# Kernel tuning notes

Hardware: AMD Instinct MI355X
Metric: run time of the kernel (lower is better)

The kernel has to match this reference:

```python
import jax, jax.numpy as jnp
import numpy as np
from jax import lax

DEPTH, HEADS, DH, DIM, M, V, NUM_EMB, D_VQ = 6, 8, 64, 512, 256, 523, 512, 64


def _ln(x, g, b):
    mu = jnp.mean(x, -1, keepdims=True)
    var = jnp.var(x, -1, keepdims=True)
    return (x - mu) * lax.rsqrt(var + 1e-5) * g + b


def _softmax_kernel(data, proj, is_query):
    # FAVOR+ positive softmax features (performer-pytorch softmax_kernel)
    dn = data * (data.shape[-1] ** -0.25)
    dd = jnp.einsum('bhld,md->bhlm', dn, proj)
    diag = 0.5 * jnp.sum(dn * dn, axis=-1, keepdims=True)
    mx = jnp.max(dd, axis=-1, keepdims=True) if is_query else jnp.max(dd)
    return jnp.exp(dd - diag - lax.stop_gradient(mx)) * (proj.shape[0] ** -0.5) + 1e-4


def _causal_linear_attn(qp, kp, v):
    # out_t = qp_t . cumsum_t(kp v^T) / (qp_t . cumsum_t(kp))
    kc = jnp.cumsum(kp, axis=2)
    den = jnp.einsum('bhlm,bhlm->bhl', qp, kc)
    kv = jnp.cumsum(jnp.einsum('bhlm,bhld->bhlmd', kp, v), axis=2)
    return jnp.einsum('bhlm,bhlmd->bhld', qp, kv) / den[..., None]


def _vq_encode(_x, conv1_w, conv1_b, conv2_w, conv2_b, codebook):
    dn = ('NCDHW', 'OIDHW', 'NCDHW')
    h = lax.conv_general_dilated(_x, conv1_w, (2, 2, 2), [(1, 1)] * 3, dimension_numbers=dn)
    h = jax.nn.relu(h + conv1_b[None, :, None, None, None])
    h = lax.conv_general_dilated(h, conv2_w, (2, 2, 2), [(1, 1)] * 3, dimension_numbers=dn)
    h = h + conv2_b[None, :, None, None, None]                 # [N, D, 4,4,4]
    z = jnp.transpose(h, (0, 2, 3, 4, 1))                      # [N, 4,4,4, D]
    flat = z.reshape(-1, z.shape[-1])
    d2 = (jnp.sum(flat * flat, 1, keepdims=True)
          - 2.0 * flat @ codebook.T
          + jnp.sum(codebook * codebook, 1)[None, :])
    inds = jnp.argmin(d2, axis=1).astype(jnp.int32)
    return inds.reshape(z.shape[:4])                           # [N, 4,4,4]


def _performer_loss(seq, tok_emb, pos_emb, proj, ln1_g, ln1_b, wq, wk, wv, wo, bo,
                    ln2_g, ln2_b, ff1_w, ff1_b, ff2_w, ff2_b, lnf_g, lnf_b,
                    logits_w, logits_b):
    inp, tgt = seq[:, :-1], seq[:, 1:]
    b, L = inp.shape
    h = tok_emb[inp] + pos_emb[:L][None]
    split = lambda t: jnp.transpose(t.reshape(b, L, HEADS, DH), (0, 2, 1, 3))
    for l in range(DEPTH):
        x1 = _ln(h, ln1_g[l], ln1_b[l])
        q, k, v = split(x1 @ wq[l]), split(x1 @ wk[l]), split(x1 @ wv[l])
        qp = _softmax_kernel(q, proj[l], True)
        kp = _softmax_kernel(k, proj[l], False)
        o = _causal_linear_attn(qp, kp, v)
        o = jnp.transpose(o, (0, 2, 1, 3)).reshape(b, L, DIM)
        h = h + o @ wo[l] + bo[l]
        x2 = _ln(h, ln2_g[l], ln2_b[l])
        h = h + jax.nn.gelu(x2 @ ff1_w[l] + ff1_b[l]) @ ff2_w[l] + ff2_b[l]
    h = _ln(h, lnf_g, lnf_b)
    logits = h @ logits_w + logits_b
    lp = jax.nn.log_softmax(logits, axis=-1)
    nll = -jnp.take_along_axis(lp, tgt[..., None], axis=-1)[..., 0]
    return jnp.mean(nll)


def setup_inputs() -> dict:
    key = jax.random.key(0)
    ks = jax.random.split(key, 24)
    n = lambda k, sh, s=0.02: (jax.random.normal(k, sh) * s).astype(jnp.float32)
    bs = 16
    return {
        'x': jax.random.normal(ks[0], (bs, 1, 16, 16, 16), jnp.float32),
        'xn': jax.random.normal(ks[1], (bs, 1, 1, 16, 16, 16), jnp.float32),
        'i': jax.random.randint(ks[2], (bs, 3), 0, V, jnp.int32),
        # frozen VQ-VAE
        'conv1_w': n(ks[3], (32, 1, 4, 4, 4), 0.1), 'conv1_b': jnp.zeros((32,), jnp.float32),
        'conv2_w': n(ks[4], (D_VQ, 32, 4, 4, 4), 0.05), 'conv2_b': jnp.zeros((D_VQ,), jnp.float32),
        'codebook': jax.random.normal(ks[5], (NUM_EMB, D_VQ), jnp.float32),
        # FAVOR+ random-feature projections (non-trainable buffer)
        'proj': jax.random.normal(ks[6], (DEPTH, M, DH), jnp.float32),
        # performer params
        'tok_emb': n(ks[7], (V, DIM)), 'pos_emb': n(ks[8], (131, DIM)),
        'ln1_g': jnp.ones((DEPTH, DIM), jnp.float32), 'ln1_b': jnp.zeros((DEPTH, DIM), jnp.float32),
        'wq': n(ks[9], (DEPTH, DIM, DIM)), 'wk': n(ks[10], (DEPTH, DIM, DIM)),
        'wv': n(ks[11], (DEPTH, DIM, DIM)), 'wo': n(ks[12], (DEPTH, DIM, DIM)),
        'bo': jnp.zeros((DEPTH, DIM), jnp.float32),
        'ln2_g': jnp.ones((DEPTH, DIM), jnp.float32), 'ln2_b': jnp.zeros((DEPTH, DIM), jnp.float32),
        'ff1_w': n(ks[13], (DEPTH, DIM, 4 * DIM)), 'ff1_b': jnp.zeros((DEPTH, 4 * DIM), jnp.float32),
        'ff2_w': n(ks[14], (DEPTH, 4 * DIM, DIM)), 'ff2_b': jnp.zeros((DEPTH, DIM), jnp.float32),
        'lnf_g': jnp.ones((DIM,), jnp.float32), 'lnf_b': jnp.zeros((DIM,), jnp.float32),
        'logits_w': n(ks[15], (DIM, V)), 'logits_b': jnp.zeros((V,), jnp.float32),
    }


def reference(x, xn, i, conv1_w, conv1_b, conv2_w, conv2_b, codebook, proj,
              tok_emb, pos_emb, ln1_g, ln1_b, wq, wk, wv, wo, bo, ln2_g, ln2_b,
              ff1_w, ff1_b, ff2_w, ff2_b, lnf_g, lnf_b, logits_w, logits_b):
    bs = x.shape[0]
    _xn = xn.reshape((-1,) + xn.shape[2:])            # (b n) c x y z
    _x = jnp.concatenate([x, _xn], axis=0)
    inds = _vq_encode(_x, conv1_w, conv1_b, conv2_w, conv2_b, codebook)
    inds_i = inds[:bs].reshape(bs, -1)                # b (x y z)
    inds_r = inds[bs:].reshape(bs, -1)                # b (n x y z)
    seq = jnp.concatenate([i.astype(jnp.int32), inds_r, inds_i], axis=1)  # [b, 131]
    return _performer_loss(seq, tok_emb, pos_emb, proj, ln1_g, ln1_b, wq, wk, wv, wo,
                           bo, ln2_g, ln2_b, ff1_w, ff1_b, ff2_w, ff2_b,
                           lnf_g, lnf_b, logits_w, logits_b)
```

## Files before the change

kernel.cpp:

```cpp
#include <hip/hip_runtime.h>

#define SEQL 130
#define LSEQ 131
#define DIMM 512
#define NHEADS 8
#define MF 256
#define VSZ 523
#define NROWS (16*SEQL)
#define NBH (16*NHEADS)
#define NBHL (NBH*SEQL)
#define QSEG 1064960

typedef __attribute__((ext_vector_type(8))) short short8;
typedef __attribute__((ext_vector_type(8))) unsigned short us8;
typedef __attribute__((ext_vector_type(4))) unsigned short us4;
typedef __attribute__((ext_vector_type(4))) float f32x4;

__device__ __forceinline__ unsigned short f2bf(float f){
  unsigned int u = __float_as_uint(f);
  u += 0x7fffu + ((u>>16)&1u);
  return (unsigned short)(u>>16);
}
__device__ __forceinline__ float bf2f(unsigned short h){
  return __uint_as_float(((unsigned int)h)<<16);
}
__device__ __forceinline__ float gelu_f(float x){
  float x3 = x*x*x;
  return 0.5f*x*(1.f+tanhf(0.7978845608028654f*(x+0.044715f*x3)));
}
__device__ __forceinline__ unsigned enc_max(float f){
  unsigned u = __float_as_uint(f);
  return (u & 0x80000000u) ? ~u : (u | 0x80000000u);
}
__device__ __forceinline__ float dec_max(unsigned k){
  unsigned u = (k>>31) ? (k & 0x7fffffffu) : ~k;
  return __uint_as_float(u);
}
__device__ __forceinline__ float blk_sum(float v){
  #pragma unroll
  for(int off=32;off;off>>=1) v += __shfl_xor(v,off);
  __shared__ float tmp_s[4];
  int t=threadIdx.x;
  if((t&63)==0) tmp_s[t>>6]=v;
  __syncthreads();
  v = tmp_s[0]+tmp_s[1]+tmp_s[2]+tmp_s[3];
  __syncthreads();
  return v;
}
__device__ __forceinline__ float blk_max(float v){
  #pragma unroll
  for(int off=32;off;off>>=1) v = fmaxf(v,__shfl_xor(v,off));
  __shared__ float tmp_m[4];
  int t=threadIdx.x;
  if((t&63)==0) tmp_m[t>>6]=v;
  __syncthreads();
  v = fmaxf(fmaxf(tmp_m[0],tmp_m[1]),fmaxf(tmp_m[2],tmp_m[3]));
  __syncthreads();
  return v;
}
__device__ __forceinline__ int tok_at(const int* __restrict__ iarr,
    const int* __restrict__ inds, int b, int p){
  if(p<3)  return iarr[b*3+p];
  if(p<67) return inds[(16+b)*64 + (p-3)];
  return inds[b*64 + (p-67)];
}

__global__ __launch_bounds__(256) void conv1_k(const float* __restrict__ x,
    const float* __restrict__ xn, const float* __restrict__ w,
    const float* __restrict__ bias, float* __restrict__ out){
  int idx = blockIdx.x*256 + threadIdx.x;
  if(idx >= 32*32*8*8*8) return;
  int ow = idx & 7, oh = (idx>>3)&7, od = (idx>>6)&7, oc = (idx>>9)&31, n = idx>>14;
  const float* xp = (n<16) ? (x + n*4096) : (xn + (n-16)*4096);
  const float* wp = w + oc*64;
  float acc = bias[oc];
  #pragma unroll
  for(int kd=0;kd<4;kd++){ int id = od*2-1+kd; if((unsigned)id>=16u) continue;
    #pragma unroll
    for(int kh=0;kh<4;kh++){ int ih = oh*2-1+kh; if((unsigned)ih>=16u) continue;
      #pragma unroll
      for(int kw=0;kw<4;kw++){ int iw = ow*2-1+kw; if((unsigned)iw>=16u) continue;
        acc += xp[(id*16+ih)*16+iw]*wp[(kd*4+kh)*4+kw];
      }}}
  out[idx] = fmaxf(acc,0.f);
}

__global__ __launch_bounds__(256) void cvt8_k(const float* __restrict__ src,
    unsigned short* __restrict__ dst, int n8){
  int i = blockIdx.x*256 + threadIdx.x;
  if(i >= n8) return;
  const float* s = src + (size_t)i*8;
  us8 u;
  #pragma unroll
  for(int j=0;j<8;j++) u[j] = f2bf(s[j]);
  *(us8*)(dst + (size_t)i*8) = u;
}

__global__ __launch_bounds__(256) void im2col_k(const float* __restrict__ c1,
    unsigned short* __restrict__ icol){
  int tid = blockIdx.x*256 + threadIdx.x;
  size_t e0 = (size_t)tid*8;
  int r = (int)(e0 >> 11);
  int k0 = (int)(e0 & 2047);
  int n = r>>6, od = (r>>4)&3, oh = (r>>2)&3, ow = r&3;
  int ic = k0>>6, kd = (k0>>4)&3, kh0 = (k0>>2)&3;
  int id = od*2 - 1 + kd;
  us8 u = {};
  if((unsigned)id < 8u){
    const float* base = c1 + (size_t)(n*32+ic)*512 + id*64;
    #pragma unroll
    for(int j=0;j<8;j++){
      int kh = kh0 + (j>>2), kw = j&3;
      int ih = oh*2 - 1 + kh, iw = ow*2 - 1 + kw;
      float v = 0.f;
      if((unsigned)ih < 8u && (unsigned)iw < 8u) v = base[ih*8 + iw];
      u[j] = f2bf(v);
    }
  }
  *(us8*)(icol + e0) = u;
}

__global__ __launch_bounds__(256) void vq_k(const float* __restrict__ z,
    const float* __restrict__ cb, int* __restrict__ inds){
  int nf = blockIdx.x;
  __shared__ float zs[64];
  int t = threadIdx.x;
  if(t<64) zs[t] = z[(size_t)nf*64 + t];
  __syncthreads();
  float best = 3.0e38f; int bi = 0;
  for(int j=t; j<512; j+=256){
    const float* cr = cb + j*64;
    float dot=0.f, nn=0.f;
    #pragma unroll 8
    for(int d=0;d<64;d++){ float cv=cr[d]; dot += zs[d]*cv; nn += cv*cv; }
    float dist = nn - 2.f*dot;
    if(dist < best){ best=dist; bi=j; }
  }
  #pragma unroll
  for(int off=32;off;off>>=1){
    float ob = __shfl_down(best,off); int oi = __shfl_down(bi,off);
    if(ob<best || (ob==best && oi<bi)){ best=ob; bi=oi; }
  }
  __shared__ float rb[4]; __shared__ int ri[4];
  if((t&63)==0){ rb[t>>6]=best; ri[t>>6]=bi; }
  __syncthreads();
  if(t==0){
    for(int wv=1;wv<4;wv++){ if(rb[wv]<best || (rb[wv]==best && ri[wv]<bi)){ best=rb[wv]; bi=ri[wv]; } }
    inds[nf]=bi;
  }
}

__global__ __launch_bounds__(256) void embed_k(const int* __restrict__ iarr,
    const int* __restrict__ inds, const float* __restrict__ tok,
    const float* __restrict__ pos, float* __restrict__ h){
  int idx = blockIdx.x*256 + threadIdx.x;
  int c = idx & 511; int row = idx >> 9;
  int b = row/SEQL, l = row - b*SEQL;
  int tk = tok_at(iarr, inds, b, l);
  h[idx] = tok[tk*DIMM + c] + pos[l*DIMM + c];
}

__global__ __launch_bounds__(256) void ln_k(const float* __restrict__ in,
    const float* __restrict__ g, const float* __restrict__ bb,
    unsigned short* __restrict__ out){
  int row = blockIdx.x; int t = threadIdx.x;
  const float* xr = in + (size_t)row*DIMM;
  float x0 = xr[t], x1 = xr[t+256];
  float s = x0+x1, ss = x0*x0 + x1*x1;
  #pragma unroll
  for(int off=32;off;off>>=1){ s += __shfl_xor(s,off); ss += __shfl_xor(ss,off); }
  __shared__ float bs[4], bss[4];
  if((t&63)==0){ bs[t>>6]=s; bss[t>>6]=ss; }
  __syncthreads();
  s = bs[0]+bs[1]+bs[2]+bs[3]; ss = bss[0]+bss[1]+bss[2]+bss[3];
  float mu = s*(1.f/512.f);
  float var = ss*(1.f/512.f) - mu*mu;
  float inv = rsqrtf(var + 1e-5f);
  out[(size_t)row*DIMM+t]     = f2bf((x0-mu)*inv*g[t]     + bb[t]);
  out[(size_t)row*DIMM+t+256] = f2bf((x1-mu)*inv*g[t+256] + bb[t+256]);
}

__global__ __launch_bounds__(256) void wprep_k(const float* __restrict__ wq_l,
    const float* __restrict__ wk_l, const float* __restrict__ wv_l,
    const float* __restrict__ wo_l, const float* __restrict__ ff1_l,
    const float* __restrict__ ff2_l,
    unsigned short* __restrict__ wqkvt, unsigned short* __restrict__ wot,
    unsigned short* __restrict__ ff1t, unsigned short* __restrict__ ff2t,
    unsigned int* __restrict__ gmaxbits){
  int bid = blockIdx.x;
  int t = threadIdx.x;
  if(bid==0 && t==0) gmaxbits[0] = 0u;
  const float* src; unsigned short* dst;
  int n0, k0, srcN, dstK;
  if(bid < 768){
    int nt = bid % 48, kt = bid / 48;
    n0 = nt*32; k0 = kt*32;
    int seg = n0 >> 9;
    src = (seg==0 ? wq_l : seg==1 ? wk_l : wv_l);
    dst = wqkvt; srcN = 512; dstK = 512;
  } else if(bid < 1024){
    int b2 = bid-768; int nt = b2 % 16, kt = b2 / 16;
    n0 = nt*32; k0 = kt*32; src = wo_l; dst = wot; srcN = 512; dstK = 512;
  } else if(bid < 2048){
    int b2 = bid-1024; int nt = b2 % 64, kt = b2 / 64;
    n0 = nt*32; k0 = kt*32; src = ff1_l; dst = ff1t; srcN = 2048; dstK = 512;
  } else {
    int b2 = bid-2048; int nt = b2 % 16, kt = b2 / 16;
    n0 = nt*32; k0 = kt*32; src = ff2_l; dst = ff2t; srcN = 512; dstK = 2048;
  }
  int srcCol0 = (bid < 768) ? (n0 & 0x1ff) : n0;
  __shared__ float tile[32][33];
  int c = t&31, r = t>>5;
  #pragma unroll
  for(int j=0;j<4;j++)
    tile[r+8*j][c] = src[(size_t)(k0+r+8*j)*srcN + srcCol0 + c];
  __syncthreads();
  #pragma unroll
  for(int j=0;j<4;j++){
    int n = n0 + r + 8*j;
    dst[(size_t)n*dstK + k0 + c] = f2bf(tile[c][r+8*j]);
  }
}

__global__ __launch_bounds__(256) void wconv_k(const float* __restrict__ W,
    unsigned short* __restrict__ dst, int K, int N){
  __shared__ float tile[32][33];
  int k0 = blockIdx.y*32, n0 = blockIdx.x*32;
  int t = threadIdx.x; int c = t&31, r = t>>5;
  #pragma unroll
  for(int j=0;j<4;j++){
    int n = n0+c;
    tile[r+8*j][c] = (n<N) ? W[(size_t)(k0+r+8*j)*N + n] : 0.f;
  }
  __syncthreads();
  #pragma unroll
  for(int j=0;j<4;j++){
    int n = n0 + r + 8*j;
    if(n<N) dst[(size_t)n*K + k0 + c] = f2bf(tile[c][r+8*j]);
  }
}

template<int MODE>
__global__ __launch_bounds__(256) void mgemm_k(const unsigned short* __restrict__ A,
    const unsigned short* __restrict__ Bt, const float* __restrict__ bias,
    float* __restrict__ Cf, unsigned short* __restrict__ Cb,
    int M, int N, int K){
  __shared__ unsigned short As[4096];
  __shared__ unsigned short Bs[4096];
  int t = threadIdx.x;
  const int m0 = blockIdx.y*64, n0 = blockIdx.x*64;
  int w = t>>6, l = t&63;
  int wr = w>>1, wc = w&1;
  f32x4 acc[2][2] = {};
  int srow = t>>2, sp = (t&3)*2;
  int arow = m0 + srow, brow = n0 + srow;
  bool aok = arow < M, bok = brow < N;
  const us8* Ap = (const us8*)(A + (size_t)arow*K + sp*8);
  const us8* Bp = (const us8*)(Bt + (size_t)brow*K + sp*8);
  unsigned short* Aw0 = As + srow*64 + (((sp  )^(srow&7))<<3);
  unsigned short* Aw1 = As + srow*64 + (((sp+1)^(srow&7))<<3);
  unsigned short* Bw0 = Bs + srow*64 + (((sp  )^(srow&7))<<3);
  unsigned short* Bw1 = Bs + srow*64 + (((sp+1)^(srow&7))<<3);
  for(int k0=0; k0<K; k0+=64){
    us8 a0={}, a1={}, b0={}, b1={};
    if(aok){ a0 = Ap[0]; a1 = Ap[1]; }
    if(bok){ b0 = Bp[0]; b1 = Bp[1]; }
    Ap += 8; Bp += 8;
    __syncthreads();
    *(us8*)Aw0 = a0; *(us8*)Aw1 = a1;
    *(us8*)Bw0 = b0; *(us8*)Bw1 = b1;
    __syncthreads();
    #pragma unroll
    for(int kk=0;kk<2;kk++){
      short8 af[2], bf[2];
      #pragma unroll
      for(int m=0;m<2;m++){
        int row = wr*32 + m*16 + (l&15);
        int slot = kk*4 + (l>>4);
        af[m] = *(const short8*)(As + row*64 + ((slot^(row&7))<<3));
      }
      #pragma unroll
      for(int n=0;n<2;n++){
        int col = wc*32 + n*16 + (l&15);
        int slot = kk*4 + (l>>4);
        bf[n] = *(const short8*)(Bs + col*64 + ((slot^(col&7))<<3));
      }
      #pragma unroll
      for(int m=0;m<2;m++)
        #pragma unroll
        for(int n=0;n<2;n++)
          acc[m][n] = __builtin_amdgcn_mfma_f32_16x16x32_bf16(af[m], bf[n], acc[m][n], 0, 0, 0);
    }
  }
  #pragma unroll
  for(int m=0;m<2;m++){
    #pragma unroll
    for(int n=0;n<2;n++){
      int col = n0 + wc*32 + n*16 + (l&15);
      #pragma unroll
      for(int i=0;i<4;i++){
        int row = m0 + wr*32 + m*16 + (l>>4)*4 + i;
        if(row < M && col < N){
          float v = acc[m][n][i];
          if(MODE==0){
            if(bias) v += bias[col];
            Cf[(size_t)row*N+col] = v;
          } else if(MODE==1){
            v *= (col < 1024) ? 0.35355339059327378f : 1.0f;
            int seg = col>>9, d0 = col&511;
            int hh = d0>>6, d = d0&63;
            int bb = row/SEQL, ll = row - bb*SEQL;
            Cb[(size_t)seg*QSEG + (((size_t)(bb*NHEADS+hh))*SEQL + ll)*64 + d] = f2bf(v);
          } else if(MODE==3){
            v += bias[col];
            Cf[(size_t)row*N+col] += v;
          } else {
            v += bias[col];
            v = gelu_f(v);
            Cb[(size_t)row*N+col] = f2bf(v);
          }
        }
      }
    }
  }
}

template<int ACC>
__global__ __launch_bounds__(256) void mgemm32_k(const unsigned short* __restrict__ A,
    const unsigned short* __restrict__ Bt, const float* __restrict__ bias,
    float* __restrict__ Cf, int N, int K){
  __shared__ unsigned short As[2048];
  __shared__ unsigned short Bs[4096];
  int t = threadIdx.x;
  const int m0 = blockIdx.y*32, n0 = blockIdx.x*64;
  int w = t>>6, l = t&63;
  int wm = w&1, wn2 = w>>1;
  f32x4 acc[2] = {};
  int srowA = t>>3, spA = t&7;
  int srowB = t>>2, spB = (t&3)*2;
  const us8* Ap = (const us8*)(A + (size_t)(m0+srowA)*K + spA*8);
  const us8* Bp = (const us8*)(Bt + (size_t)(n0+srowB)*K + spB*8);
  unsigned short* Aw  = As + srowA*64 + ((spA^(srowA&7))<<3);
  unsigned short* Bw0 = Bs + srowB*64 + (((spB  )^(srowB&7))<<3);
  unsigned short* Bw1 = Bs + srowB*64 + (((spB+1)^(srowB&7))<<3);
  for(int k0=0; k0<K; k0+=64){
    us8 a0 = Ap[0];
    us8 b0 = Bp[0], b1 = Bp[1];
    Ap += 8; Bp += 8;
    __syncthreads();
    *(us8*)Aw = a0;
    *(us8*)Bw0 = b0; *(us8*)Bw1 = b1;
    __syncthreads();
    #pragma unroll
    for(int kk=0;kk<2;kk++){
      int arow = wm*16 + (l&15);
      int slot = kk*4 + (l>>4);
      short8 af = *(const short8*)(As + arow*64 + ((slot^(arow&7))<<3));
      #pragma unroll
      for(int n=0;n<2;n++){
        int col = (wn2*2+n)*16 + (l&15);
        short8 bf = *(const short8*)(Bs + col*64 + ((slot^(col&7))<<3));
        acc[n] = __builtin_amdgcn_mfma_f32_16x16x32_bf16(af, bf, acc[n], 0, 0, 0);
      }
    }
  }
  #pragma unroll
  for(int n=0;n<2;n++){
    int col = n0 + (wn2*2+n)*16 + (l&15);
    float bv = bias[col];
    #pragma unroll
    for(int i=0;i<4;i++){
      int row = m0 + wm*16 + (l>>4)*4 + i;
      if(ACC) Cf[(size_t)row*N+col] += acc[n][i] + bv;
      else    Cf[(size_t)row*N+col]  = acc[n][i] + bv;
    }
  }
}

__global__ __launch_bounds__(256) void featA_k(const unsigned short* __restrict__ qn,
    const unsigned short* __restrict__ kn, const unsigned short* __restrict__ projl,
    unsigned short* __restrict__ qp, unsigned int* __restrict__ gmaxbits){
  int z = blockIdx.y;
  const unsigned short* dn = z ? kn : qn;
  __shared__ float uni[32*264];
  __shared__ unsigned short dns[2048];
  unsigned short* ps = (unsigned short*)uni;
  int t = threadIdx.x;
  size_t R0 = (size_t)blockIdx.x*32;
  {
    int row = t>>3, sl = t&7;
    us8 u = *(const us8*)(dn + (R0+row)*64 + sl*8);
    *(us8*)(dns + row*64 + ((sl^(row&7))<<3)) = u;
  }
  #pragma unroll
  for(int j=0;j<8;j++){
    int ridx = t + 256*j;
    int row = ridx>>3, sl = ridx&7;
    us8 u = *(const us8*)(projl + row*64 + sl*8);
    *(us8*)(ps + row*64 + ((sl^(row&7))<<3)) = u;
  }
  __syncthreads();
  int w = t>>6, l = t&63;
  int rt = w&1, cb = (w>>1)*8;
  f32x4 acc[8] = {};
  #pragma unroll
  for(int kk=0;kk<2;kk++){
    int ar = rt*16 + (l&15);
    int slot = kk*4 + (l>>4);
    short8 a = *(const short8*)(dns + ar*64 + ((slot^(ar&7))<<3));
    #pragma unroll
    for(int ct=0;ct<8;ct++){
      int br = (cb+ct)*16 + (l&15);
      short8 b = *(const short8*)(ps + br*64 + ((slot^(br&7))<<3));
      acc[ct] = __builtin_amdgcn_mfma_f32_16x16x32_bf16(a, b, acc[ct], 0, 0, 0);
    }
  }
  __syncthreads();
  #pragma unroll
  for(int ct=0;ct<8;ct++){
    int col = (cb+ct)*16 + (l&15);
    #pragma unroll
    for(int i=0;i<4;i++){
      int row = rt*16 + (l>>4)*4 + i;
      uni[row*264 + col] = acc[ct][i];
    }
  }
  __syncthreads();
  int r = t>>3, sub = t&7;
  float* rowp = uni + r*264 + sub*32;
  f32x4 v[8];
  #pragma unroll
  for(int jj=0;jj<8;jj++) v[jj] = *(const f32x4*)(rowp + jj*4);
  float m = -3.0e38f;
  #pragma unroll
  for(int jj=0;jj<8;jj++)
    #pragma unroll
    for(int i=0;i<4;i++) m = fmaxf(m, v[jj][i]);
  m = fmaxf(m, __shfl_xor(m,1));
  m = fmaxf(m, __shfl_xor(m,2));
  m = fmaxf(m, __shfl_xor(m,4));
  if(z==0){
    us8 dvu = *(const us8*)(dns + r*64 + ((sub^(r&7))<<3));
    float s2 = 0.f;
    #pragma unroll
    for(int j=0;j<8;j++){ float xx = bf2f(dvu[j]); s2 += xx*xx; }
    s2 += __shfl_xor(s2,1); s2 += __shfl_xor(s2,2); s2 += __shfl_xor(s2,4);
    float ds = 0.5f*s2;
    unsigned short* op = qp + (R0+r)*256 + sub*32;
    #pragma unroll
    for(int jj=0;jj<8;jj++){
      us4 u4;
      #pragma unroll
      for(int i=0;i<4;i++) u4[i] = f2bf(expf(v[jj][i] - ds - m)*0.0625f + 1e-4f);
      *(us4*)(op + jj*4) = u4;
    }
  } else {
    float bm = m;
    bm = fmaxf(bm, __shfl_xor(bm,8));
    bm = fmaxf(bm, __shfl_xor(bm,16));
    bm = fmaxf(bm, __shfl_xor(bm,32));
    __shared__ float wm[4];
    if(l==0) wm[w] = bm;
    __syncthreads();
    if(t==0){
      float g = fmaxf(fmaxf(wm[0],wm[1]),fmaxf(wm[2],wm[3]));
      atomicMax(gmaxbits, enc_max(g));
    }
  }
}

__global__ __launch_bounds__(256) void featB_k(const unsigned short* __restrict__ kn,
    const unsigned short* __restrict__ projl, const unsigned int* __restrict__ gmaxbits,
    unsigned short* __restrict__ kp){
  __shared__ float uni[32*264];
  __shared__ unsigned short dns[2048];
  unsigned short* ps = (unsigned short*)uni;
  int t = threadIdx.x;
  size_t R0 = (size_t)blockIdx.x*32;
  {
    int row = t>>3, sl = t&7;
    us8 u = *(const us8*)(kn + (R0+row)*64 + sl*8);
    *(us8*)(dns + row*64 + ((sl^(row&7))<<3)) = u;
  }
  #pragma unroll
  for(int j=0;j<8;j++){
    int ridx = t + 256*j;
    int row = ridx>>3, sl = ridx&7;
    us8 u = *(const us8*)(projl + row*64 + sl*8);
    *(us8*)(ps + row*64 + ((sl^(row&7))<<3)) = u;
  }
  __syncthreads();
  int w = t>>6, l = t&63;
  int rt = w&1, cb = (w>>1)*8;
  f32x4 acc[8] = {};
  #pragma unroll
  for(int kk=0;kk<2;kk++){
    int ar = rt*16 + (l&15);
    int slot = kk*4 + (l>>4);
    short8 a = *(const short8*)(dns + ar*64 + ((slot^(ar&7))<<3));
    #pragma unroll
    for(int ct=0;ct<8;ct++){
      int br = (cb+ct)*16 + (l&15);
      short8 b = *(const short8*)(ps + br*64 + ((slot^(br&7))<<3));
      acc[ct] = __builtin_amdgcn_mfma_f32_16x16x32_bf16(a, b, acc[ct], 0, 0, 0);
    }
  }
  __syncthreads();
  #pragma unroll
  for(int ct=0;ct<8;ct++){
    int col = (cb+ct)*16 + (l&15);
    #pragma unroll
    for(int i=0;i<4;i++){
      int row = rt*16 + (l>>4)*4 + i;
      uni[row*264 + col] = acc[ct][i];
    }
  }
  __syncthreads();
  float g = dec_max(gmaxbits[0]);
  int r = t>>3, sub = t&7;
  us8 dvu = *(const us8*)(dns + r*64 + ((sub^(r&7))<<3));
  float s2 = 0.f;
  #pragma unroll
  for(int j=0;j<8;j++){ float xx = bf2f(dvu[j]); s2 += xx*xx; }
  s2 += __shfl_xor(s2,1); s2 += __shfl_xor(s2,2); s2 += __shfl_xor(s2,4);
  float ds = 0.5f*s2;
  float* rowp = uni + r*264 + sub*32;
  unsigned short* op = kp + (R0+r)*256 + sub*32;
  #pragma unroll
  for(int jj=0;jj<8;jj++){
    f32x4 v = *(const f32x4*)(rowp + jj*4);
    us4 u4;
    #pragma unroll
    for(int i=0;i<4;i++) u4[i] = f2bf(expf(v[i] - ds - g)*0.0625f + 1e-4f);
    *(us4*)(op + jj*4) = u4;
  }
}

__global__ __launch_bounds__(256) void attn_k(const unsigned short* __restrict__ qp,
    const unsigned short* __restrict__ kp, const unsigned short* __restrict__ vn,
    unsigned short* __restrict__ ob){
  int qt = blockIdx.x, bh = blockIdx.y;
  int b = bh>>3, hh = bh&7;
  __shared__ unsigned short qs[32*256];
  __shared__ unsigned short ks[32*256];
  __shared__ float vs[32][68];
  __shared__ float Ss[32][33];
  __shared__ float dens[2][32];
  int t = threadIdx.x;
  int w = t>>6, l = t&63;
  int qh = w>>1, kh = w&1;
  {
    int rr = t>>3, s0 = (t&7)*4;
    int gr = qt*32 + rr;
    const us8* src = (const us8*)(qp + ((size_t)bh*SEQL + (gr<SEQL?gr:0))*256 + s0*8);
    #pragma unroll
    for(int j=0;j<4;j++){
      us8 u = {};
      if(gr<SEQL) u = src[j];
      *(us8*)(qs + rr*256 + (((s0+j)^(rr&7))<<3)) = u;
    }
  }
  if(t<64) dens[t>>5][t&31] = 0.f;
  float o[8] = {0.f,0.f,0.f,0.f,0.f,0.f,0.f,0.f};
  int orow = t>>3, od = (t&7)*8;
  for(int kt=0; kt<=qt; kt++){
    __syncthreads();
    {
      int rr = t>>3, s0 = (t&7)*4;
      int gk = kt*32 + rr;
      const us8* src = (const us8*)(kp + ((size_t)bh*SEQL + (gk<SEQL?gk:0))*256 + s0*8);
      #pragma unroll
      for(int j=0;j<4;j++){
        us8 u = {};
        if(gk<SEQL) u = src[j];
        *(us8*)(ks + rr*256 + (((s0+j)^(rr&7))<<3)) = u;
      }
      const us8* vsrc = (const us8*)(vn + ((size_t)bh*SEQL + (gk<SEQL?gk:0))*64 + od);
      us8 uv = {};
      if(gk<SEQL) uv = vsrc[0];
      #pragma unroll
      for(int i=0;i<8;i++) vs[rr][od+i] = bf2f(uv[i]);
    }
    __syncthreads();
    f32x4 sacc = {};
    #pragma unroll
    for(int kk=0;kk<8;kk++){
      int ar = qh*16 + (l&15); int slot = kk*4 + (l>>4);
      short8 a = *(const short8*)(qs + ar*256 + ((slot^(ar&7))<<3));
      int br = kh*16 + (l&15);
      short8 bb2 = *(const short8*)(ks + br*256 + ((slot^(br&7))<<3));
      sacc = __builtin_amdgcn_mfma_f32_16x16x32_bf16(a, bb2, sacc, 0, 0, 0);
    }
    int scol = kh*16 + (l&15);
    int gcol = kt*32 + scol;
    float dp[4];
    #pragma unroll
    for(int i=0;i<4;i++){
      int sr = qh*16 + (l>>4)*4 + i;
      int grw = qt*32 + sr;
      float v2 = sacc[i];
      if(gcol > grw) v2 = 0.f;
      Ss[sr][scol] = v2;
      dp[i] = v2;
    }
    #pragma unroll
    for(int off=1;off<16;off<<=1)
      #pragma unroll
      for(int i=0;i<4;i++) dp[i] += __shfl_xor(dp[i], off);
    if((l&15)==0){
      #pragma unroll
      for(int i=0;i<4;i++) dens[kh][qh*16 + (l>>4)*4 + i] += dp[i];
    }
    __syncthreads();
    #pragma unroll
    for(int k2=0;k2<32;k2++){
      float s = Ss[orow][k2];
      #pragma unroll
      for(int j=0;j<8;j++) o[j] += s*vs[k2][od+j];
    }
  }
  __syncthreads();
  int gr = qt*32 + orow;
  if(gr < SEQL){
    float inv = 1.f/(dens[0][orow] + dens[1][orow]);
    us8 u;
    #pragma unroll
    for(int j=0;j<8;j++) u[j] = f2bf(o[j]*inv);
    *(us8*)(ob + ((size_t)(b*SEQL+gr))*DIMM + hh*64 + od) = u;
  }
}

__global__ __launch_bounds__(256) void loss_k(const float* __restrict__ logits,
    const int* __restrict__ iarr, const int* __restrict__ inds,
    float* __restrict__ rnll){
  int row = blockIdx.x; int t = threadIdx.x;
  const float* lr = logits + (size_t)row*VSZ;
  float m = -3.0e38f;
  for(int j=t;j<VSZ;j+=256) m = fmaxf(m, lr[j]);
  m = blk_max(m);
  float s = 0.f;
  for(int j=t;j<VSZ;j+=256) s += expf(lr[j]-m);
  s = blk_sum(s);
  if(t==0){
    int b = row/SEQL, l = row - b*SEQL;
    int tgt = tok_at(iarr, inds, b, l+1);
    rnll[row] = (m + logf(s)) - lr[tgt];
  }
}

__global__ __launch_bounds__(256) void fin_k(const float* __restrict__ rnll,
    float* __restrict__ out){
  int t = threadIdx.x;
  float s = 0.f;
  for(int i=t;i<NROWS;i+=256) s += rnll[i];
  s = blk_sum(s);
  if(t==0) out[0] = s/(float)NROWS;
}

extern "C" void kernel_launch(void* const* d_in, const int* in_sizes, int n_in,
                              void* d_out, int out_size, void* d_ws, size_t ws_size,
                              hipStream_t stream){
  (void)in_sizes; (void)n_in; (void)out_size; (void)ws_size;
  const float* x        = (const float*)d_in[0];
  const float* xn       = (const float*)d_in[1];
  const int*   iarr     = (const int*)  d_in[2];
  const float* conv1_w  = (const float*)d_in[3];
  const float* conv1_b  = (const float*)d_in[4];
  const float* conv2_w  = (const float*)d_in[5];
  const float* conv2_b  = (const float*)d_in[6];
  const float* codebook = (const float*)d_in[7];
  const float* proj     = (const float*)d_in[8];
  const float* tok_emb  = (const float*)d_in[9];
  const float* pos_emb  = (const float*)d_in[10];
  const float* ln1_g    = (const float*)d_in[11];
  const float* ln1_b    = (const float*)d_in[12];
  const float* wq       = (const float*)d_in[13];
  const float* wk       = (const float*)d_in[14];
  const float* wv       = (const float*)d_in[15];
  const float* wo       = (const float*)d_in[16];
  const float* bo       = (const float*)d_in[17];
  const float* ln2_g    = (const float*)d_in[18];
  const float* ln2_b    = (const float*)d_in[19];
  const float* ff1_w    = (const float*)d_in[20];
  const float* ff1_b    = (const float*)d_in[21];
  const float* ff2_w    = (const float*)d_in[22];
  const float* ff2_b    = (const float*)d_in[23];
  const float* lnf_g    = (const float*)d_in[24];
  const float* lnf_b    = (const float*)d_in[25];
  const float* logits_w = (const float*)d_in[26];
  const float* logits_b = (const float*)d_in[27];

  float* wsf = (float*)d_ws;
  size_t off = 0;
  unsigned short* qp_bf = (unsigned short*)(wsf + off); off += 2129920;
  unsigned short* kp_bf = (unsigned short*)(wsf + off); off += 2129920;
  float* h = wsf + off; off += 1064960;
  unsigned short* x1b = (unsigned short*)(wsf + off); off += 532480;
  unsigned short* qkvb = (unsigned short*)(wsf + off); off += 1597440;
  unsigned short* ob  = (unsigned short*)(wsf + off); off += 532480;
  unsigned short* projb = (unsigned short*)(wsf + off); off += 49152;
  unsigned short* wqkvt = (unsigned short*)(wsf + off); off += 393216;
  unsigned short* wot   = (unsigned short*)(wsf + off); off += 131072;
  unsigned short* ff1t  = (unsigned short*)(wsf + off); off += 524288;
  unsigned short* ff2t  = (unsigned short*)(wsf + off); off += 524288;
  unsigned short* logt  = (unsigned short*)(wsf + off); off += 133888;
  unsigned short* ffmid = (unsigned short*)(wsf + off); off += 2129920;
  float* logits = wsf + off; off += 1087840;
  int* inds = (int*)(wsf + off); off += 2048;
  unsigned int* gmaxbits = (unsigned int*)(wsf + off); off += 64;
  float* rnll = wsf + off; off += 2112;

  float* c1 = logits;
  unsigned short* icol = ffmid;
  float* zbuf = (float*)qp_bf;
  unsigned short* cw2b = (unsigned short*)kp_bf;

  unsigned short* qnb = qkvb;
  unsigned short* knb = qkvb + QSEG;
  unsigned short* vnb = qkvb + 2*QSEG;

  conv1_k<<<2048,256,0,stream>>>(x, xn, conv1_w, conv1_b, c1);
  cvt8_k<<<64,256,0,stream>>>(conv2_w, cw2b, 16384);
  im2col_k<<<2048,256,0,stream>>>(c1, icol);
  mgemm32_k<0><<<dim3(1,64),256,0,stream>>>(icol, cw2b, conv2_b, zbuf, 64, 2048);
  vq_k<<<2048,256,0,stream>>>(zbuf, codebook, inds);
  embed_k<<<(NROWS*DIMM)/256,256,0,stream>>>(iarr, inds, tok_emb, pos_emb, h);
  cvt8_k<<<48,256,0,stream>>>(proj, projb, 12288);
  wconv_k<<<dim3(17,16),256,0,stream>>>(logits_w, logt, 512, 523);

  for(int l=0;l<6;l++){
    wprep_k<<<3072,256,0,stream>>>(wq + (size_t)l*262144, wk + (size_t)l*262144,
        wv + (size_t)l*262144, wo + (size_t)l*262144,
        ff1_w + (size_t)l*1048576, ff2_w + (size_t)l*1048576,
        wqkvt, wot, ff1t, ff2t, gmaxbits);
    ln_k<<<NROWS,256,0,stream>>>(h, ln1_g+l*DIMM, ln1_b+l*DIMM, x1b);
    mgemm_k<1><<<dim3(24,33),256,0,stream>>>(x1b, wqkvt, nullptr, nullptr, qkvb, NROWS, 1536, DIMM);
    featA_k<<<dim3(520,2),256,0,stream>>>(qnb, knb, projb + l*16384, qp_bf, gmaxbits);
    featB_k<<<520,256,0,stream>>>(knb, projb + l*16384, gmaxbits, kp_bf);
    attn_k<<<dim3(5,NBH),256,0,stream>>>(qp_bf, kp_bf, vnb, ob);
    mgemm32_k<1><<<dim3(8,65),256,0,stream>>>(ob, wot, bo+l*DIMM, h, DIMM, DIMM);
    ln_k<<<NROWS,256,0,stream>>>(h, ln2_g+l*DIMM, ln2_b+l*DIMM, x1b);
    mgemm_k<4><<<dim3(32,33),256,0,stream>>>(x1b, ff1t, ff1_b+l*2048, nullptr, ffmid, NROWS, 2048, DIMM);
    mgemm32_k<1><<<dim3(8,65),256,0,stream>>>(ffmid, ff2t, ff2_b+l*DIMM, h, DIMM, 2048);
  }

  ln_k<<<NROWS,256,0,stream>>>(h, lnf_g, lnf_b, x1b);
  mgemm_k<0><<<dim3(9,33),256,0,stream>>>(x1b, logt, logits_b, logits, nullptr, NROWS, VSZ, DIMM);
  loss_k<<<NROWS,256,0,stream>>>(logits, iarr, inds, rnll);
  fin_k<<<1,256,0,stream>>>(rnll, (float*)d_out);
}
```

Baseline: 787.7 us.

## Batch weight prep, double-buffer GEMMs with direct-to-LDS loads, MFMA attention PV

All six layers' weights are now converted and transposed to bf16 in a single launch before the layer loop, which removes five launches and lets the work fill the device. The GEMM kernels use global_load_lds to copy tiles straight into LDS and double-buffer them, so the next tile loads while MFMAs run on the current one, and they need one barrier per k-step instead of two. The feature kernels also use direct-to-LDS loads. The attention kernel replaces the scalar S·V loop with bf16 MFMAs by storing S and a transposed V in LDS as bf16. This costs more workspace and LDS and adds bf16 rounding of the attention scores.

New measurement: 749.4 us. 4.9% less time.

```diff
diff --git a/kernel.cpp b/kernel.cpp
--- a/kernel.cpp
+++ b/kernel.cpp
@@ -10,6 +10,7 @@
 #define NBH (16*NHEADS)
 #define NBHL (NBH*SEQL)
 #define QSEG 1064960
+#define WLAYER 3145728
 
 typedef __attribute__((ext_vector_type(8))) short short8;
 typedef __attribute__((ext_vector_type(8))) unsigned short us8;
@@ -35,6 +36,11 @@
 __device__ __forceinline__ float dec_max(unsigned k){
   unsigned u = (k>>31) ? (k & 0x7fffffffu) : ~k;
   return __uint_as_float(u);
+}
+__device__ __forceinline__ void gload16(const void* g, void* lds){
+  __builtin_amdgcn_global_load_lds(
+      (const __attribute__((address_space(1))) void*)g,
+      (__attribute__((address_space(3))) void*)lds, 16, 0, 0);
 }
 __device__ __forceinline__ float blk_sum(float v){
   #pragma unroll
@@ -180,33 +186,37 @@
   out[(size_t)row*DIMM+t+256] = f2bf((x1-mu)*inv*g[t+256] + bb[t+256]);
 }
 
-__global__ __launch_bounds__(256) void wprep_k(const float* __restrict__ wq_l,
-    const float* __restrict__ wk_l, const float* __restrict__ wv_l,
-    const float* __restrict__ wo_l, const float* __restrict__ ff1_l,
-    const float* __restrict__ ff2_l,
-    unsigned short* __restrict__ wqkvt, unsigned short* __restrict__ wot,
-    unsigned short* __restrict__ ff1t, unsigned short* __restrict__ ff2t,
+__global__ __launch_bounds__(256) void wprep_k(const float* __restrict__ wq,
+    const float* __restrict__ wk, const float* __restrict__ wv,
+    const float* __restrict__ wo, const float* __restrict__ ff1,
+    const float* __restrict__ ff2, unsigned short* __restrict__ wall,
     unsigned int* __restrict__ gmaxbits){
-  int bid = blockIdx.x;
+  int bid0 = blockIdx.x;
   int t = threadIdx.x;
-  if(bid==0 && t==0) gmaxbits[0] = 0u;
+  if(bid0==0 && t<8) gmaxbits[t] = 0u;
+  int lyr = bid0 / 3072;
+  int bid = bid0 - lyr*3072;
+  unsigned short* wl = wall + (size_t)lyr*WLAYER;
   const float* src; unsigned short* dst;
   int n0, k0, srcN, dstK;
   if(bid < 768){
     int nt = bid % 48, kt = bid / 48;
     n0 = nt*32; k0 = kt*32;
     int seg = n0 >> 9;
-    src = (seg==0 ? wq_l : seg==1 ? wk_l : wv_l);
-    dst = wqkvt; srcN = 512; dstK = 512;
+    src = (seg==0 ? wq : seg==1 ? wk : wv) + (size_t)lyr*262144;
+    dst = wl; srcN = 512; dstK = 512;
   } else if(bid < 1024){
     int b2 = bid-768; int nt = b2 % 16, kt = b2 / 16;
-    n0 = nt*32; k0 = kt*32; src = wo_l; dst = wot; srcN = 512; dstK = 512;
+    n0 = nt*32; k0 = kt*32; src = wo + (size_t)lyr*262144;
+    dst = wl + 786432; srcN = 512; dstK = 512;
   } else if(bid < 2048){
     int b2 = bid-1024; int nt = b2 % 64, kt = b2 / 64;
-    n0 = nt*32; k0 = kt*32; src = ff1_l; dst = ff1t; srcN = 2048; dstK = 512;
+    n0 = nt*32; k0 = kt*32; src = ff1 + (size_t)lyr*1048576;
+    dst = wl + 1048576; srcN = 2048; dstK = 512;
   } else {
     int b2 = bid-2048; int nt = b2 % 16, kt = b2 / 16;
-    n0 = nt*32; k0 = kt*32; src = ff2_l; dst = ff2t; srcN = 512; dstK = 2048;
+    n0 = nt*32; k0 = kt*32; src = ff2 + (size_t)lyr*1048576;
+    dst = wl + 2097152; srcN = 512; dstK = 2048;
   }
   int srcCol0 = (bid < 768) ? (n0 & 0x1ff) : n0;
   __shared__ float tile[32][33];
@@ -245,31 +255,33 @@
     const unsigned short* __restrict__ Bt, const float* __restrict__ bias,
     float* __restrict__ Cf, unsigned short* __restrict__ Cb,
     int M, int N, int K){
-  __shared__ unsigned short As[4096];
-  __shared__ unsigned short Bs[4096];
+  __shared__ __attribute__((aligned(16))) unsigned short As[2][4096];
+  __shared__ __attribute__((aligned(16))) unsigned short Bs[2][4096];
   int t = threadIdx.x;
   const int m0 = blockIdx.y*64, n0 = blockIdx.x*64;
   int w = t>>6, l = t&63;
   int wr = w>>1, wc = w&1;
   f32x4 acc[2][2] = {};
-  int srow = t>>2, sp = (t&3)*2;
-  int arow = m0 + srow, brow = n0 + srow;
-  bool aok = arow < M, bok = brow < N;
-  const us8* Ap = (const us8*)(A + (size_t)arow*K + sp*8);
-  const us8* Bp = (const us8*)(Bt + (size_t)brow*K + sp*8);
-  unsigned short* Aw0 = As + srow*64 + (((sp  )^(srow&7))<<3);
-  unsigned short* Aw1 = As + srow*64 + (((sp+1)^(srow&7))<<3);
-  unsigned short* Bw0 = Bs + srow*64 + (((sp  )^(srow&7))<<3);
-  unsigned short* Bw1 = Bs + srow*64 + (((sp+1)^(srow&7))<<3);
-  for(int k0=0; k0<K; k0+=64){
-    us8 a0={}, a1={}, b0={}, b1={};
-    if(aok){ a0 = Ap[0]; a1 = Ap[1]; }
-    if(bok){ b0 = Bp[0]; b1 = Bp[1]; }
-    Ap += 8; Bp += 8;
+  auto stage = [&](unsigned short* Ad, unsigned short* Bd, int k0){
+    #pragma unroll
+    for(int i=0;i<2;i++){
+      int c = w*2 + i;
+      int r = c*8 + (l>>3);
+      int gc = k0 + (((l&7) ^ (r&7))<<3);
+      int ar = m0 + r; if(ar >= M) ar = 0;
+      gload16(A + (size_t)ar*K + gc, Ad + c*512);
+      int br = n0 + r; if(br >= N) br = 0;
+      gload16(Bt + (size_t)br*K + gc, Bd + c*512);
+    }
+  };
+  stage(As[0], Bs[0], 0);
+  int NT = K>>6;
+  int buf = 0;
+  for(int kt=0; kt<NT; kt++){
     __syncthreads();
-    *(us8*)Aw0 = a0; *(us8*)Aw1 = a1;
-    *(us8*)Bw0 = b0; *(us8*)Bw1 = b1;
-    __syncthreads();
+    if(kt+1 < NT) stage(As[buf^1], Bs[buf^1], (kt+1)*64);
+    const unsigned short* Ab = &As[buf][0];
+    const unsigned short* Bb = &Bs[buf][0];
     #pragma unroll
     for(int kk=0;kk<2;kk++){
       short8 af[2], bf[2];
@@ -277,13 +289,13 @@
       for(int m=0;m<2;m++){
         int row = wr*32 + m*16 + (l&15);
         int slot = kk*4 + (l>>4);
-        af[m] = *(const short8*)(As + row*64 + ((slot^(row&7))<<3));
+        af[m] = *(const short8*)(Ab + row*64 + ((slot^(row&7))<<3));
       }
       #pragma unroll
       for(int n=0;n<2;n++){
         int col = wc*32 + n*16 + (l&15);
         int slot = kk*4 + (l>>4);
-        bf[n] = *(const short8*)(Bs + col*64 + ((slot^(col&7))<<3));
+        bf[n] = *(const short8*)(Bb + col*64 + ((slot^(col&7))<<3));
       }
       #pragma unroll
       for(int m=0;m<2;m++)
@@ -291,6 +303,7 @@
         for(int n=0;n<2;n++)
           acc[m][n] = __builtin_amdgcn_mfma_f32_16x16x32_bf16(af[m], bf[n], acc[m][n], 0, 0, 0);
     }
+    buf ^= 1;
   }
   #pragma unroll
   for(int m=0;m<2;m++){
@@ -329,40 +342,49 @@
 __global__ __launch_bounds__(256) void mgemm32_k(const unsigned short* __restrict__ A,
     const unsigned short* __restrict__ Bt, const float* __restrict__ bias,
     float* __restrict__ Cf, int N, int K){
-  __shared__ unsigned short As[2048];
-  __shared__ unsigned short Bs[4096];
+  __shared__ __attribute__((aligned(16))) unsigned short As[2][2048];
+  __shared__ __attribute__((aligned(16))) unsigned short Bs[2][4096];
   int t = threadIdx.x;
   const int m0 = blockIdx.y*32, n0 = blockIdx.x*64;
   int w = t>>6, l = t&63;
   int wm = w&1, wn2 = w>>1;
   f32x4 acc[2] = {};
-  int srowA = t>>3, spA = t&7;
-  int srowB = t>>2, spB = (t&3)*2;
-  const us8* Ap = (const us8*)(A + (size_t)(m0+srowA)*K + spA*8);
-  const us8* Bp = (const us8*)(Bt + (size_t)(n0+srowB)*K + spB*8);
-  unsigned short* Aw  = As + srowA*64 + ((spA^(srowA&7))<<3);
-  unsigned short* Bw0 = Bs + srowB*64 + (((spB  )^(srowB&7))<<3);
-  unsigned short* Bw1 = Bs + srowB*64 + (((spB+1)^(srowB&7))<<3);
-  for(int k0=0; k0<K; k0+=64){
-    us8 a0 = Ap[0];
-    us8 b0 = Bp[0], b1 = Bp[1];
-    Ap += 8; Bp += 8;
+  auto stage = [&](unsigned short* Ad, unsigned short* Bd, int k0){
+    {
+      int c = w;
+      int r = c*8 + (l>>3);
+      int gc = k0 + (((l&7) ^ (r&7))<<3);
+      gload16(A + (size_t)(m0+r)*K + gc, Ad + c*512);
+    }
+    #pragma unroll
+    for(int i=0;i<2;i++){
+      int c = w*2 + i;
+      int r = c*8 + (l>>3);
+      int gc = k0 + (((l&7) ^ (r&7))<<3);
+      gload16(Bt + (size_t)(n0+r)*K + gc, Bd + c*512);
+    }
+  };
+  stage(As[0], Bs[0], 0);
+  int NT = K>>6;
+  int buf = 0;
+  for(int kt=0; kt<NT; kt++){
     __syncthreads();
-    *(us8*)Aw = a0;
-    *(us8*)Bw0 = b0; *(us8*)Bw1 = b1;
-    __syncthreads();
+    if(kt+1 < NT) stage(As[buf^1], Bs[buf^1], (kt+1)*64);
+    const unsigned short* Ab = &As[buf][0];
+    const unsigned short* Bb = &Bs[buf][0];
     #pragma unroll
     for(int kk=0;kk<2;kk++){
       int arow = wm*16 + (l&15);
       int slot = kk*4 + (l>>4);
-      short8 af = *(const short8*)(As + arow*64 + ((slot^(arow&7))<<3));
+      short8 af = *(const short8*)(Ab + arow*64 + ((slot^(arow&7))<<3));
       #pragma unroll
       for(int n=0;n<2;n++){
         int col = (wn2*2+n)*16 + (l&15);
-        short8 bf = *(const short8*)(Bs + col*64 + ((slot^(col&7))<<3));
+        short8 bf = *(const short8*)(Bb + col*64 + ((slot^(col&7))<<3));
         acc[n] = __builtin_amdgcn_mfma_f32_16x16x32_bf16(af, bf, acc[n], 0, 0, 0);
       }
     }
+    buf ^= 1;
   }
   #pragma unroll
   for(int n=0;n<2;n++){
@@ -382,25 +404,24 @@
     unsigned short* __restrict__ qp, unsigned int* __restrict__ gmaxbits){
   int z = blockIdx.y;
   const unsigned short* dn = z ? kn : qn;
-  __shared__ float uni[32*264];
-  __shared__ unsigned short dns[2048];
+  __shared__ __attribute__((aligned(16))) float uni[32*264];
+  __shared__ __attribute__((aligned(16))) unsigned short dns[2048];
   unsigned short* ps = (unsigned short*)uni;
   int t = threadIdx.x;
+  int w = t>>6, l = t&63;
   size_t R0 = (size_t)blockIdx.x*32;
   {
-    int row = t>>3, sl = t&7;
-    us8 u = *(const us8*)(dn + (R0+row)*64 + sl*8);
-    *(us8*)(dns + row*64 + ((sl^(row&7))<<3)) = u;
-  }
-  #pragma unroll
-  for(int j=0;j<8;j++){
-    int ridx = t + 256*j;
-    int row = ridx>>3, sl = ridx&7;
-    us8 u = *(const us8*)(projl + row*64 + sl*8);
-    *(us8*)(ps + row*64 + ((sl^(row&7))<<3)) = u;
-  }
-  __syncthreads();
-  int w = t>>6, l = t&63;
+    int c = w; int r = c*8 + (l>>3);
+    int gc = (((l&7) ^ (r&7))<<3);
+    gload16(dn + (R0+r)*64 + gc, dns + c*512);
+  }
+  #pragma unroll
+  for(int i=0;i<8;i++){
+    int c = w*8 + i; int r = c*8 + (l>>3);
+    int gc = (((l&7) ^ (r&7))<<3);
+    gload16(projl + (size_t)r*64 + gc, ps + c*512);
+  }
+  __syncthreads();
   int rt = w&1, cb = (w>>1)*8;
   f32x4 acc[8] = {};
   #pragma unroll
@@ -472,25 +493,24 @@
 __global__ __launch_bounds__(256) void featB_k(const unsigned short* __restrict__ kn,
     const unsigned short* __restrict__ projl, const unsigned int* __restrict__ gmaxbits,
     unsigned short* __restrict__ kp){
-  __shared__ float uni[32*264];
-  __shared__ unsigned short dns[2048];
+  __shared__ __attribute__((aligned(16))) float uni[32*264];
+  __shared__ __attribute__((aligned(16))) unsigned short dns[2048];
   unsigned short* ps = (unsigned short*)uni;
   int t = threadIdx.x;
+  int w = t>>6, l = t&63;
   size_t R0 = (size_t)blockIdx.x*32;
   {
-    int row = t>>3, sl = t&7;
-    us8 u = *(const us8*)(kn + (R0+row)*64 + sl*8);
-    *(us8*)(dns + row*64 + ((sl^(row&7))<<3)) = u;
-  }
-  #pragma unroll
-  for(int j=0;j<8;j++){
-    int ridx = t + 256*j;
-    int row = ridx>>3, sl = ridx&7;
-    us8 u = *(const us8*)(projl + row*64 + sl*8);
-    *(us8*)(ps + row*64 + ((sl^(row&7))<<3)) = u;
-  }
-  __syncthreads();
-  int w = t>>6, l = t&63;
+    int c = w; int r = c*8 + (l>>3);
+    int gc = (((l&7) ^ (r&7))<<3);
+    gload16(kn + (R0+r)*64 + gc, dns + c*512);
+  }
+  #pragma unroll
+  for(int i=0;i<8;i++){
+    int c = w*8 + i; int r = c*8 + (l>>3);
+    int gc = (((l&7) ^ (r&7))<<3);
+    gload16(projl + (size_t)r*64 + gc, ps + c*512);
+  }
+  __syncthreads();
   int rt = w&1, cb = (w>>1)*8;
   f32x4 acc[8] = {};
   #pragma unroll
@@ -541,45 +561,39 @@
     unsigned short* __restrict__ ob){
   int qt = blockIdx.x, bh = blockIdx.y;
   int b = bh>>3, hh = bh&7;
-  __shared__ unsigned short qs[32*256];
-  __shared__ unsigned short ks[32*256];
-  __shared__ float vs[32][68];
-  __shared__ float Ss[32][33];
+  __shared__ __attribute__((aligned(16))) unsigned short qs[8192];
+  __shared__ __attribute__((aligned(16))) unsigned short ks[8192];
+  __shared__ __attribute__((aligned(16))) unsigned short VTs[64*34];
+  __shared__ __attribute__((aligned(16))) unsigned short Sb[32*36];
   __shared__ float dens[2][32];
   int t = threadIdx.x;
   int w = t>>6, l = t&63;
-  int qh = w>>1, kh = w&1;
-  {
-    int rr = t>>3, s0 = (t&7)*4;
-    int gr = qt*32 + rr;
-    const us8* src = (const us8*)(qp + ((size_t)bh*SEQL + (gr<SEQL?gr:0))*256 + s0*8);
-    #pragma unroll
-    for(int j=0;j<4;j++){
-      us8 u = {};
-      if(gr<SEQL) u = src[j];
-      *(us8*)(qs + rr*256 + (((s0+j)^(rr&7))<<3)) = u;
-    }
+  int qh = w>>1, nc = w&1;
+  #pragma unroll
+  for(int i=0;i<4;i++){
+    int c = w*4 + i; int r = (c<<1) + (l>>5); int sl = l&31;
+    int gc = ((sl ^ (r&7))<<3);
+    int gr = qt*32 + r; if(gr >= SEQL) gr = 0;
+    gload16(qp + ((size_t)bh*SEQL + gr)*256 + gc, qs + c*512);
   }
   if(t<64) dens[t>>5][t&31] = 0.f;
-  float o[8] = {0.f,0.f,0.f,0.f,0.f,0.f,0.f,0.f};
-  int orow = t>>3, od = (t&7)*8;
+  f32x4 oacc[2] = {};
   for(int kt=0; kt<=qt; kt++){
     __syncthreads();
+    #pragma unroll
+    for(int i=0;i<4;i++){
+      int c = w*4 + i; int r = (c<<1) + (l>>5); int sl = l&31;
+      int gc = ((sl ^ (r&7))<<3);
+      int gk = kt*32 + r; if(gk >= SEQL) gk = 0;
+      gload16(kp + ((size_t)bh*SEQL + gk)*256 + gc, ks + c*512);
+    }
     {
-      int rr = t>>3, s0 = (t&7)*4;
+      int rr = t>>3, od = (t&7)*8;
       int gk = kt*32 + rr;
-      const us8* src = (const us8*)(kp + ((size_t)bh*SEQL + (gk<SEQL?gk:0))*256 + s0*8);
-      #pragma unroll
-      for(int j=0;j<4;j++){
-        us8 u = {};
-        if(gk<SEQL) u = src[j];
-        *(us8*)(ks + rr*256 + (((s0+j)^(rr&7))<<3)) = u;
-      }
-      const us8* vsrc = (const us8*)(vn + ((size_t)bh*SEQL + (gk<SEQL?gk:0))*64 + od);
       us8 uv = {};
-      if(gk<SEQL) uv = vsrc[0];
-      #pragma unroll
-      for(int i=0;i<8;i++) vs[rr][od+i] = bf2f(uv[i]);
+      if(gk < SEQL) uv = *(const us8*)(vn + ((size_t)bh*SEQL + gk)*64 + od);
+      #pragma unroll
+      for(int j=0;j<8;j++) VTs[(od+j)*34 + rr] = uv[j];
     }
     __syncthreads();
     f32x4 sacc = {};
@@ -587,11 +601,11 @@
     for(int kk=0;kk<8;kk++){
       int ar = qh*16 + (l&15); int slot = kk*4 + (l>>4);
       short8 a = *(const short8*)(qs + ar*256 + ((slot^(ar&7))<<3));
-      int br = kh*16 + (l&15);
+      int br = nc*16 + (l&15);
       short8 bb2 = *(const short8*)(ks + br*256 + ((slot^(br&7))<<3));
       sacc = __builtin_amdgcn_mfma_f32_16x16x32_bf16(a, bb2, sacc, 0, 0, 0);
     }
-    int scol = kh*16 + (l&15);
+    int scol = nc*16 + (l&15);
     int gcol = kt*32 + scol;
     float dp[4];
     #pragma unroll
@@ -600,7 +614,7 @@
       int grw = qt*32 + sr;
       float v2 = sacc[i];
       if(gcol > grw) v2 = 0.f;
-      Ss[sr][scol] = v2;
+      Sb[sr*36 + scol] = f2bf(v2);
       dp[i] = v2;
     }
     #pragma unroll
@@ -609,24 +623,30 @@
       for(int i=0;i<4;i++) dp[i] += __shfl_xor(dp[i], off);
     if((l&15)==0){
       #pragma unroll
-      for(int i=0;i<4;i++) dens[kh][qh*16 + (l>>4)*4 + i] += dp[i];
+      for(int i=0;i<4;i++) dens[nc][qh*16 + (l>>4)*4 + i] += dp[i];
     }
     __syncthreads();
-    #pragma unroll
-    for(int k2=0;k2<32;k2++){
-      float s = Ss[orow][k2];
-      #pragma unroll
-      for(int j=0;j<8;j++) o[j] += s*vs[k2][od+j];
-    }
-  }
-  __syncthreads();
-  int gr = qt*32 + orow;
-  if(gr < SEQL){
-    float inv = 1.f/(dens[0][orow] + dens[1][orow]);
-    us8 u;
-    #pragma unroll
-    for(int j=0;j<8;j++) u[j] = f2bf(o[j]*inv);
-    *(us8*)(ob + ((size_t)(b*SEQL+gr))*DIMM + hh*64 + od) = u;
+    short8 a2 = *(const short8*)(Sb + (qh*16 + (l&15))*36 + (l>>4)*8);
+    #pragma unroll
+    for(int n2=0;n2<2;n2++){
+      int d = nc*32 + n2*16 + (l&15);
+      short8 b2 = *(const short8*)(VTs + d*34 + (l>>4)*8);
+      oacc[n2] = __builtin_amdgcn_mfma_f32_16x16x32_bf16(a2, b2, oacc[n2], 0, 0, 0);
+    }
+  }
+  __syncthreads();
+  #pragma unroll
+  for(int n2=0;n2<2;n2++){
+    int d = nc*32 + n2*16 + (l&15);
+    #pragma unroll
+    for(int i=0;i<4;i++){
+      int rit = qh*16 + (l>>4)*4 + i;
+      int gr = qt*32 + rit;
+      if(gr < SEQL){
+        float inv = 1.f/(dens[0][rit] + dens[1][rit]);
+        ob[((size_t)(b*SEQL+gr))*DIMM + hh*64 + d] = f2bf(oacc[n2][i]*inv);
+      }
+    }
   }
 }
 
@@ -699,10 +719,7 @@
   unsigned short* qkvb = (unsigned short*)(wsf + off); off += 1597440;
   unsigned short* ob  = (unsigned short*)(wsf + off); off += 532480;
   unsigned short* projb = (unsigned short*)(wsf + off); off += 49152;
-  unsigned short* wqkvt = (unsigned short*)(wsf + off); off += 393216;
-  unsigned short* wot   = (unsigned short*)(wsf + off); off += 131072;
-  unsigned short* ff1t  = (unsigned short*)(wsf + off); off += 524288;
-  unsigned short* ff2t  = (unsigned short*)(wsf + off); off += 524288;
+  unsigned short* wall  = (unsigned short*)(wsf + off); off += 9437184;
   unsigned short* logt  = (unsigned short*)(wsf + off); off += 133888;
   unsigned short* ffmid = (unsigned short*)(wsf + off); off += 2129920;
   float* logits = wsf + off; off += 1087840;
@@ -727,16 +744,18 @@
   embed_k<<<(NROWS*DIMM)/256,256,0,stream>>>(iarr, inds, tok_emb, pos_emb, h);
   cvt8_k<<<48,256,0,stream>>>(proj, projb, 12288);
   wconv_k<<<dim3(17,16),256,0,stream>>>(logits_w, logt, 512, 523);
+  wprep_k<<<18432,256,0,stream>>>(wq, wk, wv, wo, ff1_w, ff2_w, wall, gmaxbits);
 
   for(int l=0;l<6;l++){
-    wprep_k<<<3072,256,0,stream>>>(wq + (size_t)l*262144, wk + (size_t)l*262144,
-        wv + (size_t)l*262144, wo + (size_t)l*262144,
-        ff1_w + (size_t)l*1048576, ff2_w + (size_t)l*1048576,
-        wqkvt, wot, ff1t, ff2t, gmaxbits);
+    unsigned short* wl    = wall + (size_t)l*WLAYER;
+    unsigned short* wqkvt = wl;
+    unsigned short* wot   = wl + 786432;
+    unsigned short* ff1t  = wl + 1048576;
+    unsigned short* ff2t  = wl + 2097152;
     ln_k<<<NROWS,256,0,stream>>>(h, ln1_g+l*DIMM, ln1_b+l*DIMM, x1b);
     mgemm_k<1><<<dim3(24,33),256,0,stream>>>(x1b, wqkvt, nullptr, nullptr, qkvb, NROWS, 1536, DIMM);
-    featA_k<<<dim3(520,2),256,0,stream>>>(qnb, knb, projb + l*16384, qp_bf, gmaxbits);
-    featB_k<<<520,256,0,stream>>>(knb, projb + l*16384, gmaxbits, kp_bf);
+    featA_k<<<dim3(520,2),256,0,stream>>>(qnb, knb, projb + l*16384, qp_bf, gmaxbits + l);
+    featB_k<<<520,256,0,stream>>>(knb, projb + l*16384, gmaxbits + l, kp_bf);
     attn_k<<<dim3(5,NBH),256,0,stream>>>(qp_bf, kp_bf, vnb, ob);
     mgemm32_k<1><<<dim3(8,65),256,0,stream>>>(ob, wot, bo+l*DIMM, h, DIMM, DIMM);
     ln_k<<<NROWS,256,0,stream>>>(h, ln2_g+l*DIMM, ln2_b+l*DIMM, x1b);
```
